# Kernel optimization log

Hardware: AMD Instinct MI355X
Metric: run time of the kernel (lower is better)

## Reference

```python
import jax, jax.numpy as jnp
import numpy as np

B, M, K, N = 4, 2048, 4096, 4096


def setup_inputs() -> dict:
    key = jax.random.key(0)
    k1, k2, k3, k4, k5 = jax.random.split(key, 5)
    # int8 quantized activations and weights (stored as int8, like the torch buffers)
    x_q = jax.random.randint(k1, (B, M, K), -128, 127, dtype=jnp.int8)
    weight = jax.random.randint(k2, (N, K), -128, 127, dtype=jnp.int8)
    # per-token activation scales and per-output-row weight scales (symmetric quant)
    scales_x = jax.random.uniform(k3, (B, M, 1), dtype=jnp.float32) * 0.01 + 1e-4
    weight_scales = jax.random.uniform(k4, (N, 1), dtype=jnp.float32) * 0.01 + 1e-4
    bias = jax.random.normal(k5, (N,), dtype=jnp.float32)
    return {"x_q": x_q, "scales_x": scales_x, "weight": weight,
            "weight_scales": weight_scales, "bias": bias}


def reference(x_q, scales_x, weight, weight_scales, bias):
    # int8 GEMM accumulating in int32: (B*M, K) @ (K, N) with weight stored (N, K)
    acc = jnp.einsum(
        'bmk,nk->bmn',
        x_q.astype(jnp.int32), weight.astype(jnp.int32),
        preferred_element_type=jnp.int32,
    )  # [B, M, N] int32
    # symmetric dequant: row (token) scale * column (output-channel) scale, then bias
    out = acc.astype(jnp.float32) * scales_x * weight_scales[:, 0] + bias
    return out.astype(jnp.float16)
```

## Files before the change

### kernel.cpp

```cpp
#include <hip/hip_runtime.h>

typedef int v4i __attribute__((ext_vector_type(4)));

constexpr int Kdim = 4096;
constexpr int Ndim = 4096;
constexpr int MtotC = 8192;
constexpr int BM = 256;
constexpr int BN = 256;
constexpr int BKB = 128;
constexpr int NT = Kdim / BKB;

__global__ void pack_i32_to_i8(const int* __restrict__ src,
                               signed char* __restrict__ dst, size_t n4) {
    size_t i = (size_t)blockIdx.x * blockDim.x + threadIdx.x;
    size_t stride = (size_t)gridDim.x * blockDim.x;
    for (size_t j = i; j < n4; j += stride) {
        const int4 v = ((const int4*)src)[j];
        char4 c;
        c.x = (signed char)v.x; c.y = (signed char)v.y;
        c.z = (signed char)v.z; c.w = (signed char)v.w;
        ((char4*)dst)[j] = c;
    }
}

__global__ __launch_bounds__(512, 2) void i8gemm_kernel(
    const signed char* __restrict__ A,
    const signed char* __restrict__ W,
    const float* __restrict__ sx,
    const float* __restrict__ wsc,
    const float* __restrict__ bias,
    float* __restrict__ C)
{
    extern __shared__ signed char smem[];

    const int tid  = threadIdx.x;
    const int wave = tid >> 6;
    const int lane = tid & 63;
    const int wr = wave >> 2;
    const int wc = wave & 3;

    int wg = blockIdx.x;
    wg = (wg & 7) * 64 + (wg >> 3);
    const int bm = (wg & 31) * BM;
    const int bn = (wg >> 5) * BN;

    const int srow = tid >> 3;
    const int ssw  = ((tid & 7) ^ ((tid >> 3) & 7)) * 16;
    const signed char* Ag = A + (size_t)(bm + srow) * Kdim + ssw;
    const signed char* Wg = W + (size_t)(bn + srow) * Kdim + ssw;

    auto STAGE = [&](int kt, int buf) {
        signed char* dA = smem + buf * 65536 + tid * 16;
        signed char* dB = dA + 32768;
        const signed char* sA = Ag + (size_t)kt * BKB;
        const signed char* sB = Wg + (size_t)kt * BKB;
#pragma unroll
        for (int r = 0; r < 4; ++r)
            __builtin_amdgcn_global_load_lds(
                (const __attribute__((address_space(1))) void*)(sA + (size_t)r * 64 * Kdim),
                (__attribute__((address_space(3))) void*)(dA + r * 8192), 16, 0, 0);
#pragma unroll
        for (int r = 0; r < 4; ++r)
            __builtin_amdgcn_global_load_lds(
                (const __attribute__((address_space(1))) void*)(sB + (size_t)r * 64 * Kdim),
                (__attribute__((address_space(3))) void*)(dB + r * 8192), 16, 0, 0);
    };

    const int frow = lane & 15;
    const int fsl  = lane >> 4;
    const int xr   = frow & 7;
    const int s0   = ((fsl)     ^ xr) * 16;
    const int s1   = ((4 + fsl) ^ xr) * 16;
    const int aoff = (wr * 128 + frow) * BKB;
    const int boff = (wc * 64  + frow) * BKB;

    v4i acc[8][4];
#pragma unroll
    for (int f = 0; f < 8; ++f)
#pragma unroll
        for (int g = 0; g < 4; ++g)
#pragma unroll
            for (int e = 0; e < 4; ++e) acc[f][g][e] = 0;

    auto COMPUTE = [&](int buf) {
        const signed char* bA = smem + buf * 65536 + aoff;
        const signed char* bB = smem + buf * 65536 + 32768 + boff;
        v4i av[8], bv[4];
#pragma unroll
        for (int g = 0; g < 4; ++g) bv[g] = *(const v4i*)(bB + g * 2048 + s0);
#pragma unroll
        for (int f = 0; f < 8; ++f) av[f] = *(const v4i*)(bA + f * 2048 + s0);
        __builtin_amdgcn_s_setprio(1);
#pragma unroll
        for (int f = 0; f < 8; ++f)
#pragma unroll
            for (int g = 0; g < 4; ++g)
                acc[f][g] = __builtin_amdgcn_mfma_i32_16x16x64_i8(av[f], bv[g], acc[f][g], 0, 0, 0);
        __builtin_amdgcn_s_setprio(0);
#pragma unroll
        for (int g = 0; g < 4; ++g) bv[g] = *(const v4i*)(bB + g * 2048 + s1);
#pragma unroll
        for (int f = 0; f < 8; ++f) av[f] = *(const v4i*)(bA + f * 2048 + s1);
        __builtin_amdgcn_s_setprio(1);
#pragma unroll
        for (int f = 0; f < 8; ++f)
#pragma unroll
            for (int g = 0; g < 4; ++g)
                acc[f][g] = __builtin_amdgcn_mfma_i32_16x16x64_i8(av[f], bv[g], acc[f][g], 0, 0, 0);
        __builtin_amdgcn_s_setprio(0);
    };

    STAGE(0, 0);
    STAGE(1, 1);
    asm volatile("s_waitcnt vmcnt(8)" ::: "memory");
    __builtin_amdgcn_s_barrier();

    for (int t = 0; t < NT; ++t) {
        const int cur = t & 1;
        COMPUTE(cur);
        __builtin_amdgcn_sched_barrier(0);
        asm volatile("s_waitcnt lgkmcnt(0)" ::: "memory");
        __builtin_amdgcn_s_barrier();
        if (t + 2 < NT) {
            STAGE(t + 2, cur);
            asm volatile("s_waitcnt vmcnt(8)" ::: "memory");
            __builtin_amdgcn_s_barrier();
        } else if (t + 1 < NT) {
            asm volatile("s_waitcnt vmcnt(0)" ::: "memory");
            __builtin_amdgcn_s_barrier();
        }
    }

    const int orow0 = bm + wr * 128;
    const int ocol0 = bn + wc * 64;
    float wsv[4], bvv[4];
#pragma unroll
    for (int g = 0; g < 4; ++g) {
        const int col = ocol0 + g * 16 + frow;
        wsv[g] = wsc[col];
        bvv[g] = bias[col];
    }
#pragma unroll
    for (int f = 0; f < 8; ++f) {
#pragma unroll
        for (int jr = 0; jr < 4; ++jr) {
            const int row = orow0 + f * 16 + fsl * 4 + jr;
            const float s = sx[row];
#pragma unroll
            for (int g = 0; g < 4; ++g) {
                const int col = ocol0 + g * 16 + frow;
                C[(size_t)row * Ndim + col] = (float)acc[f][g][jr] * s * wsv[g] + bvv[g];
            }
        }
    }
}

extern "C" void kernel_launch(void* const* d_in, const int* in_sizes, int n_in,
                              void* d_out, int out_size, void* d_ws, size_t ws_size,
                              hipStream_t stream) {
    (void)in_sizes; (void)n_in; (void)out_size; (void)ws_size;
    const int*   x_q  = (const int*)d_in[0];
    const float* sx   = (const float*)d_in[1];
    const int*   w_q  = (const int*)d_in[2];
    const float* wsc  = (const float*)d_in[3];
    const float* bias = (const float*)d_in[4];
    float* out = (float*)d_out;

    signed char* x8 = (signed char*)d_ws;
    signed char* w8 = x8 + (size_t)MtotC * Kdim;

    const size_t nx = (size_t)MtotC * Kdim;
    const size_t nw = (size_t)Ndim * Kdim;

    pack_i32_to_i8<<<2048, 256, 0, stream>>>(x_q, x8, nx / 4);
    pack_i32_to_i8<<<1024, 256, 0, stream>>>(w_q, w8, nw / 4);

    static bool attr_set = false;
    if (!attr_set) {
        hipFuncSetAttribute((const void*)i8gemm_kernel,
                            hipFuncAttributeMaxDynamicSharedMemorySize, 131072);
        attr_set = true;
    }

    const int nwg = (MtotC / BM) * (Ndim / BN);
    i8gemm_kernel<<<nwg, 512, 131072, stream>>>(x8, w8, sx, wsc, bias, out);
}
```

Baseline: 190.9 us.

## Restructure int8 GEMM main loop into half-K phases with interleaved LDS staging

Splits each 128-byte K tile into two 64-byte halves stored in separate LDS regions with a new XOR swizzle, and reorganizes the main loop into four phases that interleave global-to-LDS prefetches with MFMA blocks of 16 instructions each. This aims to overlap memory traffic with compute more finely and reduce register pressure by holding only 4 A fragments at a time. The block-to-tile mapping is changed to 8x8 supertiles for L2 reuse, and the two pack kernels are merged into one launch. It adds many more barriers per tile, which may cost synchronisation overhead.

Result: no change. 189.5 us (-0.7%).

```diff
diff --git a/kernel.cpp b/kernel.cpp
--- a/kernel.cpp
+++ b/kernel.cpp
@@ -10,16 +10,27 @@
 constexpr int BKB = 128;
 constexpr int NT = Kdim / BKB;
 
-__global__ void pack_i32_to_i8(const int* __restrict__ src,
-                               signed char* __restrict__ dst, size_t n4) {
+__global__ void pack_i32_to_i8(const int* __restrict__ xq, const int* __restrict__ wq,
+                               signed char* __restrict__ x8, signed char* __restrict__ w8,
+                               size_t nx4, size_t nw4) {
     size_t i = (size_t)blockIdx.x * blockDim.x + threadIdx.x;
     size_t stride = (size_t)gridDim.x * blockDim.x;
-    for (size_t j = i; j < n4; j += stride) {
-        const int4 v = ((const int4*)src)[j];
-        char4 c;
-        c.x = (signed char)v.x; c.y = (signed char)v.y;
-        c.z = (signed char)v.z; c.w = (signed char)v.w;
-        ((char4*)dst)[j] = c;
+    size_t tot = nx4 + nw4;
+    for (size_t j = i; j < tot; j += stride) {
+        if (j < nx4) {
+            const int4 v = ((const int4*)xq)[j];
+            char4 c;
+            c.x = (signed char)v.x; c.y = (signed char)v.y;
+            c.z = (signed char)v.z; c.w = (signed char)v.w;
+            ((char4*)x8)[j] = c;
+        } else {
+            const size_t k = j - nx4;
+            const int4 v = ((const int4*)wq)[k];
+            char4 c;
+            c.x = (signed char)v.x; c.y = (signed char)v.y;
+            c.z = (signed char)v.z; c.w = (signed char)v.w;
+            ((char4*)w8)[k] = c;
+        }
     }
 }
 
@@ -39,40 +50,23 @@
     const int wr = wave >> 2;
     const int wc = wave & 3;
 
-    int wg = blockIdx.x;
-    wg = (wg & 7) * 64 + (wg >> 3);
-    const int bm = (wg & 31) * BM;
-    const int bn = (wg >> 5) * BN;
-
-    const int srow = tid >> 3;
-    const int ssw  = ((tid & 7) ^ ((tid >> 3) & 7)) * 16;
-    const signed char* Ag = A + (size_t)(bm + srow) * Kdim + ssw;
-    const signed char* Wg = W + (size_t)(bn + srow) * Kdim + ssw;
-
-    auto STAGE = [&](int kt, int buf) {
-        signed char* dA = smem + buf * 65536 + tid * 16;
-        signed char* dB = dA + 32768;
-        const signed char* sA = Ag + (size_t)kt * BKB;
-        const signed char* sB = Wg + (size_t)kt * BKB;
-#pragma unroll
-        for (int r = 0; r < 4; ++r)
-            __builtin_amdgcn_global_load_lds(
-                (const __attribute__((address_space(1))) void*)(sA + (size_t)r * 64 * Kdim),
-                (__attribute__((address_space(3))) void*)(dA + r * 8192), 16, 0, 0);
-#pragma unroll
-        for (int r = 0; r < 4; ++r)
-            __builtin_amdgcn_global_load_lds(
-                (const __attribute__((address_space(1))) void*)(sB + (size_t)r * 64 * Kdim),
-                (__attribute__((address_space(3))) void*)(dB + r * 8192), 16, 0, 0);
-    };
+    const int xr_ = blockIdx.x & 7;
+    const int idx = blockIdx.x >> 3;
+    const int bm = ((xr_ & 3) * 8 + (idx & 7)) * BM;
+    const int bn = ((xr_ >> 2) * 8 + (idx >> 3)) * BN;
+
+    const int srow_in = wave * 16 + (lane >> 2);
+    const int sslotp  = lane & 3;
+    const int gslot   = sslotp ^ ((srow_in >> 1) & 3);
+    const signed char* Ag = A + (size_t)(bm + srow_in) * Kdim + gslot * 16;
+    const signed char* Wg = W + (size_t)(bn + srow_in) * Kdim + gslot * 16;
+    const int sdst = srow_in * 64 + sslotp * 16;
 
     const int frow = lane & 15;
     const int fsl  = lane >> 4;
-    const int xr   = frow & 7;
-    const int s0   = ((fsl)     ^ xr) * 16;
-    const int s1   = ((4 + fsl) ^ xr) * 16;
-    const int aoff = (wr * 128 + frow) * BKB;
-    const int boff = (wc * 64  + frow) * BKB;
+    const int rsw  = ((fsl ^ ((frow >> 1) & 3)) << 4);
+    const int aro  = (wr * 128 + frow) * 64 + rsw;
+    const int bro  = 16384 + (wc * 64 + frow) * 64 + rsw;
 
     v4i acc[8][4];
 #pragma unroll
@@ -82,54 +76,75 @@
 #pragma unroll
             for (int e = 0; e < 4; ++e) acc[f][g][e] = 0;
 
-    auto COMPUTE = [&](int buf) {
-        const signed char* bA = smem + buf * 65536 + aoff;
-        const signed char* bB = smem + buf * 65536 + 32768 + boff;
-        v4i av[8], bv[4];
-#pragma unroll
-        for (int g = 0; g < 4; ++g) bv[g] = *(const v4i*)(bB + g * 2048 + s0);
-#pragma unroll
-        for (int f = 0; f < 8; ++f) av[f] = *(const v4i*)(bA + f * 2048 + s0);
-        __builtin_amdgcn_s_setprio(1);
-#pragma unroll
-        for (int f = 0; f < 8; ++f)
-#pragma unroll
-            for (int g = 0; g < 4; ++g)
-                acc[f][g] = __builtin_amdgcn_mfma_i32_16x16x64_i8(av[f], bv[g], acc[f][g], 0, 0, 0);
-        __builtin_amdgcn_s_setprio(0);
-#pragma unroll
-        for (int g = 0; g < 4; ++g) bv[g] = *(const v4i*)(bB + g * 2048 + s1);
-#pragma unroll
-        for (int f = 0; f < 8; ++f) av[f] = *(const v4i*)(bA + f * 2048 + s1);
-        __builtin_amdgcn_s_setprio(1);
-#pragma unroll
-        for (int f = 0; f < 8; ++f)
-#pragma unroll
-            for (int g = 0; g < 4; ++g)
-                acc[f][g] = __builtin_amdgcn_mfma_i32_16x16x64_i8(av[f], bv[g], acc[f][g], 0, 0, 0);
-        __builtin_amdgcn_s_setprio(0);
-    };
-
-    STAGE(0, 0);
-    STAGE(1, 1);
+#define STG(KT, HALF, RB) do {                                                         \
+    __builtin_amdgcn_global_load_lds(                                                  \
+        (const __attribute__((address_space(1))) void*)(Ag + (size_t)(RB) * Kdim + (KT) * BKB + (HALF) * 64), \
+        (__attribute__((address_space(3))) void*)(smem + ((KT) & 1) * 65536 + (HALF) * 32768 + (RB) * 64 + sdst), \
+        16, 0, 0);                                                                     \
+    __builtin_amdgcn_global_load_lds(                                                  \
+        (const __attribute__((address_space(1))) void*)(Wg + (size_t)(RB) * Kdim + (KT) * BKB + (HALF) * 64), \
+        (__attribute__((address_space(3))) void*)(smem + ((KT) & 1) * 65536 + (HALF) * 32768 + 16384 + (RB) * 64 + sdst), \
+        16, 0, 0);                                                                     \
+} while (0)
+
+#define BAR   __builtin_amdgcn_s_barrier()
+#define LGKM0 asm volatile("s_waitcnt lgkmcnt(0)" ::: "memory")
+#define PRIO1 __builtin_amdgcn_s_setprio(1)
+#define PRIO0 __builtin_amdgcn_s_setprio(0)
+
+#define PH_READ_AB(HALF) do {                                                          \
+    _Pragma("unroll") for (int g_ = 0; g_ < 4; ++g_)                                   \
+        bv[g_] = *(const v4i*)(bufb + (HALF) * 32768 + bro + g_ * 1024);               \
+    _Pragma("unroll") for (int f_ = 0; f_ < 4; ++f_)                                   \
+        av[f_] = *(const v4i*)(bufb + (HALF) * 32768 + aro + f_ * 1024);               \
+} while (0)
+
+#define PH_READ_A4(HALF) do {                                                          \
+    _Pragma("unroll") for (int f_ = 0; f_ < 4; ++f_)                                   \
+        av[f_] = *(const v4i*)(bufb + (HALF) * 32768 + aro + (4 + f_) * 1024);         \
+} while (0)
+
+#define MFMA_BLOCK(FB) do {                                                            \
+    _Pragma("unroll") for (int f_ = 0; f_ < 4; ++f_)                                   \
+    _Pragma("unroll") for (int g_ = 0; g_ < 4; ++g_)                                   \
+        acc[(FB) + f_][g_] = __builtin_amdgcn_mfma_i32_16x16x64_i8(                    \
+            av[f_], bv[g_], acc[(FB) + f_][g_], 0, 0, 0);                              \
+} while (0)
+
+#define TILE_BODY(U, DOS12, DOS34, W2STR, DOW4, W4STR) do {                            \
+    signed char* bufb = smem + ((U) & 1) * 65536;                                      \
+    v4i av[4], bv[4];                                                                  \
+                                                        \
+    PH_READ_AB(0);                                                                     \
+    if (DOS12) STG((U) + 1, 1, 0);                                                     \
+    BAR; LGKM0; PRIO1; MFMA_BLOCK(0); PRIO0; BAR;                                      \
+                                                        \
+    PH_READ_A4(0);                                                                     \
+    if (DOS12) STG((U) + 1, 1, 128);                                                   \
+    BAR; LGKM0; PRIO1; MFMA_BLOCK(4); PRIO0;                                           \
+    asm volatile("s_waitcnt " W2STR ::: "memory"); BAR;                                \
+                                                        \
+    PH_READ_AB(1);                                                                     \
+    if (DOS34) STG((U) + 2, 0, 0);                                                     \
+    BAR; LGKM0; PRIO1; MFMA_BLOCK(0); PRIO0; BAR;                                      \
+                                                        \
+    PH_READ_A4(1);                                                                     \
+    if (DOS34) STG((U) + 2, 0, 128);                                                   \
+    BAR; LGKM0; PRIO1; MFMA_BLOCK(4); PRIO0;                                           \
+    if (DOW4) { asm volatile("s_waitcnt " W4STR ::: "memory"); }                       \
+    BAR;                                                                               \
+} while (0)
+
+    STG(0, 0, 0);  STG(0, 0, 128);
+    STG(0, 1, 0);  STG(0, 1, 128);
+    STG(1, 0, 0);  STG(1, 0, 128);
     asm volatile("s_waitcnt vmcnt(8)" ::: "memory");
-    __builtin_amdgcn_s_barrier();
-
-    for (int t = 0; t < NT; ++t) {
-        const int cur = t & 1;
-        COMPUTE(cur);
-        __builtin_amdgcn_sched_barrier(0);
-        asm volatile("s_waitcnt lgkmcnt(0)" ::: "memory");
-        __builtin_amdgcn_s_barrier();
-        if (t + 2 < NT) {
-            STAGE(t + 2, cur);
-            asm volatile("s_waitcnt vmcnt(8)" ::: "memory");
-            __builtin_amdgcn_s_barrier();
-        } else if (t + 1 < NT) {
-            asm volatile("s_waitcnt vmcnt(0)" ::: "memory");
-            __builtin_amdgcn_s_barrier();
-        }
-    }
+    BAR;
+
+    for (int u = 0; u < NT - 2; ++u)
+        TILE_BODY(u, true, true, "vmcnt(8)", true, "vmcnt(8)");
+    TILE_BODY(NT - 2, true,  false, "vmcnt(8)", true,  "vmcnt(4)");
+    TILE_BODY(NT - 1, false, false, "vmcnt(0)", false, "vmcnt(0)");
 
     const int orow0 = bm + wr * 128;
     const int ocol0 = bn + wc * 64;
@@ -153,6 +168,15 @@
             }
         }
     }
+#undef STG
+#undef BAR
+#undef LGKM0
+#undef PRIO1
+#undef PRIO0
+#undef PH_READ_AB
+#undef PH_READ_A4
+#undef MFMA_BLOCK
+#undef TILE_BODY
 }
 
 extern "C" void kernel_launch(void* const* d_in, const int* in_sizes, int n_in,
@@ -172,8 +196,7 @@
     const size_t nx = (size_t)MtotC * Kdim;
     const size_t nw = (size_t)Ndim * Kdim;
 
-    pack_i32_to_i8<<<2048, 256, 0, stream>>>(x_q, x8, nx / 4);
-    pack_i32_to_i8<<<1024, 256, 0, stream>>>(w_q, w8, nw / 4);
+    pack_i32_to_i8<<<3072, 256, 0, stream>>>(x_q, w_q, x8, w8, nx / 4, nw / 4);
 
     static bool attr_set = false;
     if (!attr_set) {
```
